# Optimization experiments

Hardware: AMD Instinct MI355X
Metric: run time of the kernel (lower is better)

The kernel has to match this reference:

```python
import jax, jax.numpy as jnp
import numpy as np

N_NODES = 50000
N_EDGES = 800000
D_IN = 64
D_OUT = 64


def setup_inputs() -> dict:
    key = jax.random.key(0)
    ks = jax.random.split(key, 5)
    feat = jax.random.normal(ks[0], (N_NODES, D_IN), dtype=jnp.float32)
    src = jax.random.randint(ks[1], (N_EDGES,), 0, N_NODES, dtype=jnp.int64)
    dst = jax.random.randint(ks[2], (N_EDGES,), 0, N_NODES, dtype=jnp.int64)
    # Xavier-uniform-ish scale for weights
    lim = float(np.sqrt(6.0 / (D_IN + D_OUT)) * np.sqrt(2.0))
    W_neigh = jax.random.uniform(ks[3], (D_OUT, D_IN), dtype=jnp.float32, minval=-lim, maxval=lim)
    W_self = jax.random.uniform(ks[4], (D_OUT, D_IN), dtype=jnp.float32, minval=-lim, maxval=lim)
    b_self = jnp.zeros((D_OUT,), dtype=jnp.float32)
    return {"feat": feat, "src": src, "dst": dst,
            "W_neigh": W_neigh, "W_self": W_self, "b_self": b_self}


def reference(feat, src, dst, W_neigh, W_self, b_self):
    # srcdata = fc_neigh(feat_src)  -> [N, D_OUT]
    srcdata = feat @ W_neigh.T
    # A_div.T @ srcdata == mean of transformed source feats over in-edges per dst.
    # deg[j] = A.sum(0)[j]; column scaling by 1/deg then transpose-SpMM.
    agg = jax.ops.segment_sum(srcdata[src], dst, num_segments=N_NODES)  # [N, D_OUT]
    deg = jax.ops.segment_sum(jnp.ones_like(dst, dtype=srcdata.dtype), dst,
                              num_segments=N_NODES)  # [N]
    # Zero-degree columns stay zero in the sparse product (no stored nonzeros).
    dstdata = jnp.where(deg[:, None] > 0, agg / jnp.maximum(deg, 1.0)[:, None], 0.0)
    # rst = fc_self(feat_dst) + dstdata ; feat_dst = feat[:N_dst] = feat (square A)
    return feat @ W_self.T + b_self + dstdata
```

## Files before the change

### kernel.cpp

```cpp
#include <hip/hip_runtime.h>

#define N_NODES 50000
#define N_EDGES 800000
#define D 64
#define RB 128
#define NBUCK 391
#define CAP 3072
#define PAD 16
#define NFEATBLK 3125
#define GN 64
#define NCHUNK 196
#define CHUNK 4096
#define ALD 68

typedef __attribute__((ext_vector_type(8))) __bf16 bf16x8;
typedef __attribute__((ext_vector_type(4))) float f32x4;
typedef __attribute__((ext_vector_type(2))) float f32x2;

__device__ inline unsigned f2bf(float f) {
    unsigned b = __builtin_bit_cast(unsigned, f);
    b += 0x7fffu + ((b >> 16) & 1u);
    return b >> 16;
}

__device__ inline void acc16(float* acc, uint4 v) {
    f32x2 a;
    a = __builtin_amdgcn_cvt_pk_f32_fp8((int)v.x, false); acc[0]  += a.x; acc[1]  += a.y;
    a = __builtin_amdgcn_cvt_pk_f32_fp8((int)v.x, true);  acc[2]  += a.x; acc[3]  += a.y;
    a = __builtin_amdgcn_cvt_pk_f32_fp8((int)v.y, false); acc[4]  += a.x; acc[5]  += a.y;
    a = __builtin_amdgcn_cvt_pk_f32_fp8((int)v.y, true);  acc[6]  += a.x; acc[7]  += a.y;
    a = __builtin_amdgcn_cvt_pk_f32_fp8((int)v.z, false); acc[8]  += a.x; acc[9]  += a.y;
    a = __builtin_amdgcn_cvt_pk_f32_fp8((int)v.z, true);  acc[10] += a.x; acc[11] += a.y;
    a = __builtin_amdgcn_cvt_pk_f32_fp8((int)v.w, false); acc[12] += a.x; acc[13] += a.y;
    a = __builtin_amdgcn_cvt_pk_f32_fp8((int)v.w, true);  acc[14] += a.x; acc[15] += a.y;
}

__global__ __launch_bounds__(256) void prep_scatter_kernel(
        const float* __restrict__ feat, const float* __restrict__ Wn, const float* __restrict__ Ws,
        const int* __restrict__ src, const int* __restrict__ dst,
        unsigned short* __restrict__ fb, unsigned* __restrict__ fq,
        unsigned short* __restrict__ wnb, unsigned short* __restrict__ wsb,
        int* __restrict__ bcursor, unsigned int* __restrict__ ebuf) {
    __shared__ int cntB[NBUCK];
    __shared__ int baseB[NBUCK];
    int b = blockIdx.x;
    int t = threadIdx.x;
    if (b < NFEATBLK) {
        int i = b * 256 + t;
        float4 v = ((const float4*)feat)[i];
        uint2 o;
        o.x = f2bf(v.x) | (f2bf(v.y) << 16);
        o.y = f2bf(v.z) | (f2bf(v.w) << 16);
        ((uint2*)fb)[i] = o;
        int q = __builtin_amdgcn_cvt_pk_fp8_f32(v.x, v.y, 0, false);
        q = __builtin_amdgcn_cvt_pk_fp8_f32(v.z, v.w, q, true);
        fq[i] = (unsigned)q;
    } else if (b == NFEATBLK) {
        for (int i = t; i < D * D; i += 256) {
            wnb[i] = (unsigned short)f2bf(Wn[i]);
            wsb[i] = (unsigned short)f2bf(Ws[i]);
        }
    } else {
        int chunk = b - NFEATBLK - 1;
        for (int i = t; i < NBUCK; i += 256) cntB[i] = 0;
        __syncthreads();
        int e0 = chunk * CHUNK;
#pragma unroll
        for (int h = 0; h < 2; ++h) {
            int s_[8], bk_[8], dl_[8];
#pragma unroll
            for (int k = 0; k < 8; ++k) {
                int e = e0 + (h * 8 + k) * 256 + t;
                if (e < N_EDGES) {
                    int dv = dst[e];
                    s_[k] = src[e];
                    bk_[k] = dv >> 7;
                    dl_[k] = dv & (RB - 1);
                    atomicAdd(&cntB[bk_[k]], 1);
                } else bk_[k] = -1;
            }
            if (h == 0) {
            }
            (void)s_; (void)dl_;
        }
        __syncthreads();
        for (int i = t; i < NBUCK; i += 256) {
            int c = cntB[i];
            baseB[i] = c ? atomicAdd(&bcursor[i * PAD], c) : 0;
        }
        __syncthreads();
#pragma unroll
        for (int k = 0; k < 16; ++k) {
            int e = e0 + k * 256 + t;
            if (e < N_EDGES) {
                int dv = dst[e];
                int bk = dv >> 7, dl = dv & (RB - 1);
                int pos = atomicAdd(&baseB[bk], 1);
                if (pos < CAP)
                    ebuf[(size_t)bk * CAP + pos] = (unsigned)src[e] | ((unsigned)dl << 16);
            }
        }
    }
}

__global__ __launch_bounds__(256) void gather_mfma_kernel(
        const unsigned short* __restrict__ fb, const unsigned char* __restrict__ fq,
        const int* __restrict__ bcursor, const unsigned int* __restrict__ ebuf,
        const unsigned short* __restrict__ wsb, const unsigned short* __restrict__ wnb,
        const float* __restrict__ bias, float* __restrict__ out) {
    __shared__ int cnt[RB];
    __shared__ int cur[RB];
    __shared__ int sorted[CAP];
    __shared__ float agg[GN * ALD];
    int t = threadIdx.x;
    int bk = blockIdx.x >> 1;
    int half = blockIdx.x & 1;
    int s0 = bk * CAP;
    int n = bcursor[bk * PAD];
    if (n > CAP) n = CAP;
    if (t < RB) cnt[t] = 0;
    __syncthreads();
    for (int i = t; i < n; i += 256) atomicAdd(&cnt[ebuf[s0 + i] >> 16], 1);
    __syncthreads();
    int c = (t < RB) ? cnt[t] : 0;
    if (t < RB) cur[t] = c;
    __syncthreads();
    for (int d = 1; d < RB; d <<= 1) {
        int v = (t < RB && t >= d) ? cur[t - d] : 0;
        __syncthreads();
        if (t < RB) cur[t] += v;
        __syncthreads();
    }
    if (t < RB) cur[t] -= c;
    __syncthreads();
    for (int i = t; i < n; i += 256) {
        unsigned r = ebuf[s0 + i];
        int p = atomicAdd(&cur[r >> 16], 1);
        sorted[p] = (int)(r & 0xFFFFu);
    }
    __syncthreads();
    int ns = t >> 2, p = t & 3;
    int dl = half * GN + ns;
    int dg = cnt[dl];
    int start = cur[dl] - dg;
    float acc[16];
#pragma unroll
    for (int j = 0; j < 16; ++j) acc[j] = 0.f;
    const unsigned char* fqp = fq + p * 16;
    int i = 0;
    for (; i + 4 <= dg; i += 4) {
        int id0 = sorted[start + i + 0];
        int id1 = sorted[start + i + 1];
        int id2 = sorted[start + i + 2];
        int id3 = sorted[start + i + 3];
        uint4 v0 = *(const uint4*)(fqp + (size_t)id0 * D);
        uint4 v1 = *(const uint4*)(fqp + (size_t)id1 * D);
        uint4 v2 = *(const uint4*)(fqp + (size_t)id2 * D);
        uint4 v3 = *(const uint4*)(fqp + (size_t)id3 * D);
        acc16(acc, v0); acc16(acc, v1); acc16(acc, v2); acc16(acc, v3);
    }
    for (; i < dg; ++i) {
        int id = sorted[start + i];
        uint4 v = *(const uint4*)(fqp + (size_t)id * D);
        acc16(acc, v);
    }
    float inv = (dg > 0) ? 1.0f / (float)dg : 0.f;
#pragma unroll
    for (int j = 0; j < 16; j += 4) {
        float4 o = make_float4(acc[j] * inv, acc[j + 1] * inv, acc[j + 2] * inv, acc[j + 3] * inv);
        *(float4*)(&agg[ns * ALD + p * 16 + j]) = o;
    }
    __syncthreads();
    int r0 = blockIdx.x * GN;
    int w = t >> 6, lane = t & 63;
    int m = lane & 15, quad = lane >> 4;
    int row = r0 + 16 * w + m;
    int rowA = row < N_NODES ? row : N_NODES - 1;
    bf16x8 aS0 = *(const bf16x8*)(fb + (size_t)rowA * D + 0  + quad * 8);
    bf16x8 aS1 = *(const bf16x8*)(fb + (size_t)rowA * D + 32 + quad * 8);
    bf16x8 aA0, aA1;
#pragma unroll
    for (int j = 0; j < 8; ++j) {
        aA0[j] = (__bf16)agg[(16 * w + m) * ALD + 0  + quad * 8 + j];
        aA1[j] = (__bf16)agg[(16 * w + m) * ALD + 32 + quad * 8 + j];
    }
#pragma unroll
    for (int tt = 0; tt < 4; ++tt) {
        int nn = 16 * tt + m;
        bf16x8 bS0 = *(const bf16x8*)(wsb + (size_t)nn * D + 0  + quad * 8);
        bf16x8 bS1 = *(const bf16x8*)(wsb + (size_t)nn * D + 32 + quad * 8);
        bf16x8 bN0 = *(const bf16x8*)(wnb + (size_t)nn * D + 0  + quad * 8);
        bf16x8 bN1 = *(const bf16x8*)(wnb + (size_t)nn * D + 32 + quad * 8);
        f32x4 cc = {0.f, 0.f, 0.f, 0.f};
        cc = __builtin_amdgcn_mfma_f32_16x16x32_bf16(aS0, bS0, cc, 0, 0, 0);
        cc = __builtin_amdgcn_mfma_f32_16x16x32_bf16(aS1, bS1, cc, 0, 0, 0);
        cc = __builtin_amdgcn_mfma_f32_16x16x32_bf16(aA0, bN0, cc, 0, 0, 0);
        cc = __builtin_amdgcn_mfma_f32_16x16x32_bf16(aA1, bN1, cc, 0, 0, 0);
        float bv = bias[16 * tt + m];
#pragma unroll
        for (int reg = 0; reg < 4; ++reg) {
            int orow = r0 + 16 * w + quad * 4 + reg;
            if (orow < N_NODES)
                out[(size_t)orow * D + 16 * tt + m] = cc[reg] + bv;
        }
    }
}

extern "C" void kernel_launch(void* const* d_in, const int* in_sizes, int n_in,
                              void* d_out, int out_size, void* d_ws, size_t ws_size,
                              hipStream_t stream) {
    const float* feat  = (const float*)d_in[0];
    const int*   src   = (const int*)d_in[1];
    const int*   dst   = (const int*)d_in[2];
    const float* Wn    = (const float*)d_in[3];
    const float* Wself = (const float*)d_in[4];
    const float* bself = (const float*)d_in[5];
    float* out = (float*)d_out;

    unsigned short* featb = (unsigned short*)d_ws;
    unsigned*       featq = (unsigned*)(featb + (size_t)N_NODES * D);
    unsigned short* wnb   = (unsigned short*)(featq + (size_t)N_NODES * D / 4);
    unsigned short* wsb   = wnb + D * D;
    unsigned int*   ebuf  = (unsigned int*)(wsb + D * D);
    int* bcursor = (int*)(ebuf + (size_t)NBUCK * CAP);

    hipMemsetAsync(bcursor, 0, (size_t)NBUCK * PAD * sizeof(int), stream);

    prep_scatter_kernel<<<NFEATBLK + 1 + NCHUNK, 256, 0, stream>>>(
        feat, Wn, Wself, src, dst, featb, featq, wnb, wsb, bcursor, ebuf);
    gather_mfma_kernel<<<2 * NBUCK, 256, 0, stream>>>(
        featb, (const unsigned char*)featq, bcursor, ebuf, wsb, wnb, bself, out);
}
```

Before: 120.1 us.

## Drop bf16 feature copy, read fp32 feat directly, and keep edge records in registers

Removes the bf16 copy of the feature matrix from the prep kernel; the gather kernel now loads fp32 rows for the self term and converts them to bf16 in registers. The scatter phase drops the useless first counting loop, caches bucket and record values in registers, and skips the second global read of src/dst. Scatter blocks are also placed before the feature-quantisation blocks so the latency-bound atomic work is dispatched first. This cuts a 6.4MB write plus its reread in exchange for a wider 12.8MB fp32 read during the MFMA stage.

New measurement: 114.2 us. 4.9% less time.

```diff
diff --git a/kernel.cpp b/kernel.cpp
--- a/kernel.cpp
+++ b/kernel.cpp
@@ -38,73 +38,58 @@
 __global__ __launch_bounds__(256) void prep_scatter_kernel(
         const float* __restrict__ feat, const float* __restrict__ Wn, const float* __restrict__ Ws,
         const int* __restrict__ src, const int* __restrict__ dst,
-        unsigned short* __restrict__ fb, unsigned* __restrict__ fq,
+        unsigned* __restrict__ fq,
         unsigned short* __restrict__ wnb, unsigned short* __restrict__ wsb,
         int* __restrict__ bcursor, unsigned int* __restrict__ ebuf) {
     __shared__ int cntB[NBUCK];
     __shared__ int baseB[NBUCK];
     int b = blockIdx.x;
     int t = threadIdx.x;
-    if (b < NFEATBLK) {
-        int i = b * 256 + t;
-        float4 v = ((const float4*)feat)[i];
-        uint2 o;
-        o.x = f2bf(v.x) | (f2bf(v.y) << 16);
-        o.y = f2bf(v.z) | (f2bf(v.w) << 16);
-        ((uint2*)fb)[i] = o;
-        int q = __builtin_amdgcn_cvt_pk_fp8_f32(v.x, v.y, 0, false);
-        q = __builtin_amdgcn_cvt_pk_fp8_f32(v.z, v.w, q, true);
-        fq[i] = (unsigned)q;
-    } else if (b == NFEATBLK) {
-        for (int i = t; i < D * D; i += 256) {
-            wnb[i] = (unsigned short)f2bf(Wn[i]);
-            wsb[i] = (unsigned short)f2bf(Ws[i]);
-        }
-    } else {
-        int chunk = b - NFEATBLK - 1;
+    if (b < NCHUNK) {
         for (int i = t; i < NBUCK; i += 256) cntB[i] = 0;
         __syncthreads();
-        int e0 = chunk * CHUNK;
-#pragma unroll
-        for (int h = 0; h < 2; ++h) {
-            int s_[8], bk_[8], dl_[8];
-#pragma unroll
-            for (int k = 0; k < 8; ++k) {
-                int e = e0 + (h * 8 + k) * 256 + t;
-                if (e < N_EDGES) {
-                    int dv = dst[e];
-                    s_[k] = src[e];
-                    bk_[k] = dv >> 7;
-                    dl_[k] = dv & (RB - 1);
-                    atomicAdd(&cntB[bk_[k]], 1);
-                } else bk_[k] = -1;
-            }
-            if (h == 0) {
-            }
-            (void)s_; (void)dl_;
-        }
-        __syncthreads();
-        for (int i = t; i < NBUCK; i += 256) {
-            int c = cntB[i];
-            baseB[i] = c ? atomicAdd(&bcursor[i * PAD], c) : 0;
-        }
-        __syncthreads();
+        int e0 = b * CHUNK;
+        int rec_[16], bk_[16];
 #pragma unroll
         for (int k = 0; k < 16; ++k) {
             int e = e0 + k * 256 + t;
             if (e < N_EDGES) {
                 int dv = dst[e];
-                int bk = dv >> 7, dl = dv & (RB - 1);
-                int pos = atomicAdd(&baseB[bk], 1);
+                bk_[k] = dv >> 7;
+                rec_[k] = src[e] | ((dv & (RB - 1)) << 16);
+                atomicAdd(&cntB[bk_[k]], 1);
+            } else bk_[k] = -1;
+        }
+        __syncthreads();
+        for (int i = t; i < NBUCK; i += 256) {
+            int c = cntB[i];
+            baseB[i] = c ? atomicAdd(&bcursor[i * PAD], c) : 0;
+        }
+        __syncthreads();
+#pragma unroll
+        for (int k = 0; k < 16; ++k) {
+            if (bk_[k] >= 0) {
+                int pos = atomicAdd(&baseB[bk_[k]], 1);
                 if (pos < CAP)
-                    ebuf[(size_t)bk * CAP + pos] = (unsigned)src[e] | ((unsigned)dl << 16);
+                    ebuf[(size_t)bk_[k] * CAP + pos] = (unsigned)rec_[k];
             }
         }
+    } else if (b < NCHUNK + NFEATBLK) {
+        int i = (b - NCHUNK) * 256 + t;
+        float4 v = ((const float4*)feat)[i];
+        int q = __builtin_amdgcn_cvt_pk_fp8_f32(v.x, v.y, 0, false);
+        q = __builtin_amdgcn_cvt_pk_fp8_f32(v.z, v.w, q, true);
+        fq[i] = (unsigned)q;
+    } else {
+        for (int i = t; i < D * D; i += 256) {
+            wnb[i] = (unsigned short)f2bf(Wn[i]);
+            wsb[i] = (unsigned short)f2bf(Ws[i]);
+        }
     }
 }
 
 __global__ __launch_bounds__(256) void gather_mfma_kernel(
-        const unsigned short* __restrict__ fb, const unsigned char* __restrict__ fq,
+        const float* __restrict__ feat, const unsigned char* __restrict__ fq,
         const int* __restrict__ bcursor, const unsigned int* __restrict__ ebuf,
         const unsigned short* __restrict__ wsb, const unsigned short* __restrict__ wnb,
         const float* __restrict__ bias, float* __restrict__ out) {
@@ -176,9 +161,16 @@
     int m = lane & 15, quad = lane >> 4;
     int row = r0 + 16 * w + m;
     int rowA = row < N_NODES ? row : N_NODES - 1;
-    bf16x8 aS0 = *(const bf16x8*)(fb + (size_t)rowA * D + 0  + quad * 8);
-    bf16x8 aS1 = *(const bf16x8*)(fb + (size_t)rowA * D + 32 + quad * 8);
-    bf16x8 aA0, aA1;
+    const float* fr = feat + (size_t)rowA * D + quad * 8;
+    float4 f0 = *(const float4*)(fr + 0);
+    float4 f1 = *(const float4*)(fr + 4);
+    float4 f2 = *(const float4*)(fr + 32);
+    float4 f3 = *(const float4*)(fr + 36);
+    bf16x8 aS0, aS1, aA0, aA1;
+    aS0[0] = (__bf16)f0.x; aS0[1] = (__bf16)f0.y; aS0[2] = (__bf16)f0.z; aS0[3] = (__bf16)f0.w;
+    aS0[4] = (__bf16)f1.x; aS0[5] = (__bf16)f1.y; aS0[6] = (__bf16)f1.z; aS0[7] = (__bf16)f1.w;
+    aS1[0] = (__bf16)f2.x; aS1[1] = (__bf16)f2.y; aS1[2] = (__bf16)f2.z; aS1[3] = (__bf16)f2.w;
+    aS1[4] = (__bf16)f3.x; aS1[5] = (__bf16)f3.y; aS1[6] = (__bf16)f3.z; aS1[7] = (__bf16)f3.w;
 #pragma unroll
     for (int j = 0; j < 8; ++j) {
         aA0[j] = (__bf16)agg[(16 * w + m) * ALD + 0  + quad * 8 + j];
@@ -217,8 +209,7 @@
     const float* bself = (const float*)d_in[5];
     float* out = (float*)d_out;
 
-    unsigned short* featb = (unsigned short*)d_ws;
-    unsigned*       featq = (unsigned*)(featb + (size_t)N_NODES * D);
+    unsigned*       featq = (unsigned*)d_ws;
     unsigned short* wnb   = (unsigned short*)(featq + (size_t)N_NODES * D / 4);
     unsigned short* wsb   = wnb + D * D;
     unsigned int*   ebuf  = (unsigned int*)(wsb + D * D);
@@ -226,8 +217,8 @@
 
     hipMemsetAsync(bcursor, 0, (size_t)NBUCK * PAD * sizeof(int), stream);
 
-    prep_scatter_kernel<<<NFEATBLK + 1 + NCHUNK, 256, 0, stream>>>(
-        feat, Wn, Wself, src, dst, featb, featq, wnb, wsb, bcursor, ebuf);
+    prep_scatter_kernel<<<NCHUNK + NFEATBLK + 1, 256, 0, stream>>>(
+        feat, Wn, Wself, src, dst, featq, wnb, wsb, bcursor, ebuf);
     gather_mfma_kernel<<<2 * NBUCK, 256, 0, stream>>>(
-        featb, (const unsigned char*)featq, bcursor, ebuf, wsb, wnb, bself, out);
-}
+        feat, (const unsigned char*)featq, bcursor, ebuf, wsb, wnb, bself, out);
+}
```
